# Kernel tuning notes

Hardware: AMD Instinct MI355X
Metric: run time of the kernel (lower is better)

The kernel has to match this reference:

```python
import math
import jax, jax.numpy as jnp
import numpy as np

DIM = 1024
MAX_LEN = 5000
SPLIT_TOKEN = 49


def _make_pe(max_len, dim):
    # Sinusoidal PE, interleaved sin/cos exactly as pe[:,0::2]=sin, pe[:,1::2]=cos.
    pos = jnp.arange(max_len, dtype=jnp.float32)[:, None]                       # [L,1]
    div = jnp.exp(jnp.arange(0, dim, 2, dtype=jnp.float32) * (-(math.log(10000.0) / dim)))
    ang = pos * div                                                             # [L, dim/2]
    pe = jnp.stack([jnp.sin(ang), jnp.cos(ang)], axis=-1).reshape(max_len, dim)
    return pe[:, None, :]                                                       # [L,1,dim]


def setup_inputs() -> dict:
    key = jax.random.key(0)
    k1, k2 = jax.random.split(key)
    S, B = 4096, 8
    emb = jax.random.normal(k1, (S, B, DIM), dtype=jnp.float32)
    src_org = jax.random.randint(k2, (S, B, 1), 0, 100, dtype=jnp.int64 if jax.config.jax_enable_x64 else jnp.int32).astype(jnp.int32)
    # avoid split token at position 0 (torch code has a negative-slice quirk there)
    src_org = src_org.at[0].set(1)
    pe = _make_pe(MAX_LEN, DIM)
    return {"emb": emb, "src_org": src_org, "pe": pe}


def _doc_segments(src_org):
    # Vectorized replica of the per-column Python loop in the torch module.
    # doc[t] = number of split tokens at positions <= t, EXCEPT positions
    # immediately preceding a split, which the loop leaves at 0 (slice end is
    # split_idx - 1, exclusive).
    m = (src_org[:, :, 0] == SPLIT_TOKEN)                    # [S,B] bool
    cum = jnp.cumsum(m.astype(jnp.float32), axis=0)          # inclusive cumsum
    m_next = jnp.concatenate([m[1:], jnp.zeros_like(m[:1])], axis=0)
    doc = jnp.where(m_next, 0.0, cum)                        # [S,B]
    return doc[:, :, None]                                   # [S,B,1], float32 like torch.zeros


def reference(emb, src_org, pe):
    S = emb.shape[0]
    doc_emb = _doc_segments(src_org)          # computed by the torch forward (then unused)
    out = emb * math.sqrt(DIM) + pe[:S]       # step=None path; dropout is identity in eval
    return out, doc_emb
```

## Files before the change

### kernel.cpp

```cpp
#include <hip/hip_runtime.h>


constexpr int S_LEN   = 4096;
constexpr int B_COLS  = 8;
constexpr int DIM     = 1024;
constexpr int SPLIT   = 49;
constexpr int THREADS = 256;
constexpr int EW_BLOCKS = 2048;

__global__ __launch_bounds__(THREADS)
void pe_fused_kernel(const float* __restrict__ emb,
                     const int*   __restrict__ src,
                     const float* __restrict__ pe,
                     float* __restrict__ out,
                     float* __restrict__ doc)
{
    if (blockIdx.x < EW_BLOCKS) {
        const float scale = 32.0f;
        const size_t n4     = (size_t)S_LEN * B_COLS * DIM / 4;
        const size_t stride = (size_t)EW_BLOCKS * THREADS;
        const float4* __restrict__ emb4 = reinterpret_cast<const float4*>(emb);
        float4* __restrict__ out4       = reinterpret_cast<float4*>(out);

        for (size_t i = (size_t)blockIdx.x * THREADS + threadIdx.x; i < n4; i += stride) {
            const size_t i0 = i << 2;
            const size_t s  = i0 >> 13;
            const size_t d  = i0 & (size_t)(DIM - 1);
            float4 e = emb4[i];
            float4 p = *reinterpret_cast<const float4*>(pe + s * DIM + d);
            float4 o;
            o.x = fmaf(e.x, scale, p.x);
            o.y = fmaf(e.y, scale, p.y);
            o.z = fmaf(e.z, scale, p.z);
            o.w = fmaf(e.w, scale, p.w);
            out4[i] = o;
        }
    } else {
        const int b = blockIdx.x - EW_BLOCKS;
        const int t = threadIdx.x;
        constexpr int PER = S_LEN / THREADS;
        const int base = t * PER;

        int m[PER + 1];
        #pragma unroll
        for (int j = 0; j <= PER; ++j) {
            const int s = base + j;
            m[j] = (s < S_LEN && src[s * B_COLS + b] == SPLIT) ? 1 : 0;
        }

        int local = 0;
        #pragma unroll
        for (int j = 0; j < PER; ++j) local += m[j];

        int v = local;
        #pragma unroll
        for (int off = 1; off < 64; off <<= 1) {
            const int u = __shfl_up(v, off, 64);
            if ((t & 63) >= off) v += u;
        }

        __shared__ int wsum[THREADS / 64];
        if ((t & 63) == 63) wsum[t >> 6] = v;
        __syncthreads();

        int excl = v - local;
        for (int w = 0; w < (t >> 6); ++w) excl += wsum[w];

        int cum = excl;
        #pragma unroll
        for (int j = 0; j < PER; ++j) {
            cum += m[j];
            doc[(base + j) * B_COLS + b] = m[j + 1] ? 0.0f : (float)cum;
        }
    }
}

extern "C" void kernel_launch(void* const* d_in, const int* in_sizes, int n_in,
                              void* d_out, int out_size, void* d_ws, size_t ws_size,
                              hipStream_t stream) {
    const float* emb = (const float*)d_in[0];
    const int*   src = (const int*)d_in[1];
    const float* pe  = (const float*)d_in[2];

    float* out = (float*)d_out;
    float* doc = out + (size_t)S_LEN * B_COLS * DIM;

    pe_fused_kernel<<<EW_BLOCKS + B_COLS, THREADS, 0, stream>>>(emb, src, pe, out, doc);
}
```

Before: 251.7 us.

## Map one block per sequence row, reuse PE across batch, nontemporal streaming

Replaces the grid-stride elementwise loop with one block per sequence position. Each thread loads one PE vector once and reuses it for all 8 batch columns, issuing 8 independent loads up front for memory-level parallelism. Emb loads and out stores use nontemporal hints so they do not pollute the cache. The aim is to cut redundant PE reads and index arithmetic, at the cost of more, smaller blocks.

```diff
diff --git a/kernel.cpp b/kernel.cpp
--- a/kernel.cpp
+++ b/kernel.cpp
@@ -6,37 +6,44 @@
 constexpr int DIM     = 1024;
 constexpr int SPLIT   = 49;
 constexpr int THREADS = 256;
-constexpr int EW_BLOCKS = 2048;
+
+typedef float f32x4 __attribute__((ext_vector_type(4)));
 
 __global__ __launch_bounds__(THREADS)
-void pe_fused_kernel(const float* __restrict__ emb,
-                     const int*   __restrict__ src,
-                     const float* __restrict__ pe,
-                     float* __restrict__ out,
-                     float* __restrict__ doc)
+void pe_row_kernel(const float* __restrict__ emb,
+                   const int*   __restrict__ src,
+                   const float* __restrict__ pe,
+                   float* __restrict__ out,
+                   float* __restrict__ doc)
 {
-    if (blockIdx.x < EW_BLOCKS) {
+    if (blockIdx.x < S_LEN) {
+        const int s = blockIdx.x;
+        const int t = threadIdx.x;
         const float scale = 32.0f;
-        const size_t n4     = (size_t)S_LEN * B_COLS * DIM / 4;
-        const size_t stride = (size_t)EW_BLOCKS * THREADS;
-        const float4* __restrict__ emb4 = reinterpret_cast<const float4*>(emb);
-        float4* __restrict__ out4       = reinterpret_cast<float4*>(out);
 
-        for (size_t i = (size_t)blockIdx.x * THREADS + threadIdx.x; i < n4; i += stride) {
-            const size_t i0 = i << 2;
-            const size_t s  = i0 >> 13;
-            const size_t d  = i0 & (size_t)(DIM - 1);
-            float4 e = emb4[i];
-            float4 p = *reinterpret_cast<const float4*>(pe + s * DIM + d);
-            float4 o;
-            o.x = fmaf(e.x, scale, p.x);
-            o.y = fmaf(e.y, scale, p.y);
-            o.z = fmaf(e.z, scale, p.z);
-            o.w = fmaf(e.w, scale, p.w);
-            out4[i] = o;
+        const f32x4* __restrict__ emb4 = reinterpret_cast<const f32x4*>(emb);
+        const f32x4* __restrict__ pe4  = reinterpret_cast<const f32x4*>(pe);
+        f32x4* __restrict__ out4       = reinterpret_cast<f32x4*>(out);
+
+        const f32x4 p = pe4[(size_t)s * (DIM / 4) + t];
+        const size_t base = (size_t)s * (B_COLS * DIM / 4) + t;
+
+        f32x4 e[B_COLS];
+        #pragma unroll
+        for (int b = 0; b < B_COLS; ++b)
+            e[b] = __builtin_nontemporal_load(&emb4[base + (size_t)b * (DIM / 4)]);
+
+        #pragma unroll
+        for (int b = 0; b < B_COLS; ++b) {
+            f32x4 o;
+            o.x = fmaf(e[b].x, scale, p.x);
+            o.y = fmaf(e[b].y, scale, p.y);
+            o.z = fmaf(e[b].z, scale, p.z);
+            o.w = fmaf(e[b].w, scale, p.w);
+            __builtin_nontemporal_store(o, &out4[base + (size_t)b * (DIM / 4)]);
         }
     } else {
-        const int b = blockIdx.x - EW_BLOCKS;
+        const int b = blockIdx.x - S_LEN;
         const int t = threadIdx.x;
         constexpr int PER = S_LEN / THREADS;
         const int base = t * PER;
@@ -85,5 +92,5 @@
     float* out = (float*)d_out;
     float* doc = out + (size_t)S_LEN * B_COLS * DIM;
 
-    pe_fused_kernel<<<EW_BLOCKS + B_COLS, THREADS, 0, stream>>>(emb, src, pe, out, doc);
+    pe_row_kernel<<<S_LEN + B_COLS, THREADS, 0, stream>>>(emb, src, pe, out, doc);
 }
```

After: 239.4 us. -4.9%, faster.
